# Performance work log

Hardware: AMD Instinct MI355X
Metric: run time of the kernel (lower is better)

## Reference

```python
import jax, jax.numpy as jnp
import numpy as np

N, F, H, EMB, R, E, B = 100000, 128, 128, 64, 3, 1600000, 1024


def rgcn_conv(x, edge_src, edge_dst, edge_type, W_rel, W_root, b):
    # PyG RGCNConv with aggr='mean': out_i = x_i @ W_root + b + sum_r mean_{j in N_r(i)} x_j @ W_r
    n = x.shape[0]
    r = W_rel.shape[0]
    xr = jnp.einsum('nf,rfh->rnh', x, W_rel)            # [R,N,H] per-relation transform
    msg = xr[edge_type, edge_src]                       # [E,H] gather per edge
    seg = edge_type.astype(jnp.int32) * n + edge_dst    # fused (rel, dst) segment id
    agg = jax.ops.segment_sum(msg, seg, num_segments=r * n).reshape(r, n, -1)
    cnt = jax.ops.segment_sum(jnp.ones((msg.shape[0],), msg.dtype), seg, num_segments=r * n)
    cnt = cnt.reshape(r, n, 1)
    agg = agg / jnp.maximum(cnt, 1.0)
    return agg.sum(0) + x @ W_root + b


def setup_inputs() -> dict:
    key = jax.random.key(0)
    ks = jax.random.split(key, 16)
    s = 0.05
    return {
        'x': jax.random.normal(ks[0], (N, F), jnp.float32),
        'edge_src': jax.random.randint(ks[1], (E,), 0, N, jnp.int32),
        'edge_dst': jax.random.randint(ks[2], (E,), 0, N, jnp.int32),
        'edge_type': jax.random.randint(ks[3], (E,), 0, R, jnp.int32),
        'edge_attr': jax.random.uniform(ks[4], (E, 2), jnp.float32),
        'nest': jax.random.randint(ks[5], (B,), 0, N, jnp.int32),
        'food': jax.random.randint(ks[6], (B,), 0, N, jnp.int32),
        'W_rel1': jax.random.normal(ks[7], (R, F, H), jnp.float32) * s,
        'W_root1': jax.random.normal(ks[8], (F, H), jnp.float32) * s,
        'b1': jnp.zeros((H,), jnp.float32),
        'W_rel2': jax.random.normal(ks[9], (R, H, EMB), jnp.float32) * s,
        'W_root2': jax.random.normal(ks[10], (H, EMB), jnp.float32) * s,
        'b2': jnp.zeros((EMB,), jnp.float32),
        'fc_W': jax.random.normal(ks[11], (2 * EMB, H), jnp.float32) * s,
        'fc_b': jnp.zeros((H,), jnp.float32),
    }


def reference(x, edge_src, edge_dst, edge_type, edge_attr, nest, food,
              W_rel1, W_root1, b1, W_rel2, W_root2, b2, fc_W, fc_b):
    # distance binning (computed in the original forward but unused downstream)
    d = edge_attr[:, 0]
    dmin, dmax = d.min(), d.max()
    bin_size = (dmax - dmin) / 3
    binned = jnp.clip(jnp.floor((d - dmin) / bin_size), 0, 2)
    del binned

    h1 = jax.nn.relu(rgcn_conv(x, edge_src, edge_dst, edge_type, W_rel1, W_root1, b1))
    node = rgcn_conv(h1, edge_src, edge_dst, edge_type, W_rel2, W_root2, b2)  # [N,EMB]
    pair = jnp.concatenate([node[nest], node[food]], axis=-1)  # [B, 2*EMB]
    return jnp.tanh(pair @ fc_W + fc_b)
```

## Files before the change

kernel.cpp:

```cpp
#include <hip/hip_runtime.h>
#include <stdint.h>

typedef unsigned short u16;
typedef __attribute__((ext_vector_type(8))) short short8;
typedef __attribute__((ext_vector_type(4))) float f32x4;
typedef __attribute__((ext_vector_type(2))) float f32x2;
typedef __attribute__((ext_vector_type(4))) unsigned int u32x4;

#define N_NODES 100000
#define RREL    3
#define NEDGE   1600000
#define NPAIR   1024
#define NSEG    (RREL * N_NODES)

#define EPB   4096
#define NBLK  ((NEDGE + EPB - 1) / EPB)
#define DPB   512
#define NBIN  ((N_NODES + DPB - 1) / DPB)
#define LSEG  (DPB * RREL)
#define CAP   12288

#define PREP_TW   384
#define PREP_CAST (N_NODES * 128 / 4 / 256)

__device__ __forceinline__ float bflo(unsigned int u) {
    union { unsigned int u; float f; } c; c.u = u << 16; return c.f;
}
__device__ __forceinline__ float bfhi(unsigned int u) {
    union { unsigned int u; float f; } c; c.u = u & 0xffff0000u; return c.f;
}
__device__ __forceinline__ u16 f2bf(float f) {
    union { float f; unsigned int u; } c; c.f = f;
    unsigned int u = c.u;
    u += 0x7fffu + ((u >> 16) & 1u);
    return (u16)(u >> 16);
}

__device__ __forceinline__ void async_copy16(const u16* g, u16* l) {
    __builtin_amdgcn_global_load_lds(
        (const __attribute__((address_space(1))) unsigned int*)g,
        (__attribute__((address_space(3))) unsigned int*)l,
        16, 0, 0);
}

__global__ __launch_bounds__(256) void prep_kernel(const int* __restrict__ es,
                                                   const int* __restrict__ ed,
                                                   const int* __restrict__ et,
                                                   int* __restrict__ gpos,
                                                   unsigned int* __restrict__ binned,
                                                   const float* __restrict__ x,
                                                   u16* __restrict__ xb,
                                                   const float* __restrict__ Wrel1,
                                                   const float* __restrict__ Wroot1,
                                                   const float* __restrict__ Wrel2,
                                                   const float* __restrict__ Wroot2,
                                                   u16* __restrict__ Wt1,
                                                   u16* __restrict__ Wt2) {
    __shared__ int h[NBIN];
    __shared__ int base[NBIN];
    int b = blockIdx.x, t = threadIdx.x;
    if (b < NBLK) {
        for (int i = t; i < NBIN; i += 256) h[i] = 0;
        __syncthreads();
        int e0 = b * EPB;
        int e1 = e0 + EPB; if (e1 > NEDGE) e1 = NEDGE;
        for (int i = e0 + t; i < e1; i += 256)
            atomicAdd(&h[ed[i] >> 9], 1);
        __syncthreads();
        for (int i = t; i < NBIN; i += 256) {
            int c = h[i];
            base[i] = c ? atomicAdd(&gpos[i], c) : 0;
            h[i] = 0;
        }
        __syncthreads();
        for (int i = e0 + t; i < e1; i += 256) {
            int d = ed[i];
            int bin = d >> 9;
            unsigned int pk = ((unsigned int)es[i] << 11) | (unsigned int)((d & 511) * 3 + et[i]);
            int off = atomicAdd(&h[bin], 1);
            binned[(size_t)bin * CAP + base[bin] + off] = pk;
        }
    } else if (b < NBLK + PREP_TW) {
        int idx = (b - NBLK) * 256 + t;
        if (idx < 128 * 512) {
            int n = idx >> 9, k = idx & 511;
            float v = (k < 384) ? Wrel1[(size_t)k * 128 + n] : Wroot1[(size_t)(k - 384) * 128 + n];
            Wt1[idx] = f2bf(v);
        } else {
            int j = idx - 128 * 512;
            if (j < 256 * 128) {
                int n = j >> 7, k = j & 127;
                float v = (n < 192) ? Wrel2[((size_t)(n >> 6) * 128 + k) * 64 + (n & 63)]
                                    : Wroot2[(size_t)k * 64 + (n - 192)];
                Wt2[j] = f2bf(v);
            }
        }
    } else {
        int i = (b - NBLK - PREP_TW) * 256 + t;
        f32x4 v = __builtin_nontemporal_load(&((const f32x4*)x)[i]);
        uint2 o;
        o.x = ((unsigned int)f2bf(v.y) << 16) | (unsigned int)f2bf(v.x);
        o.y = ((unsigned int)f2bf(v.w) << 16) | (unsigned int)f2bf(v.z);
        ((uint2*)xb)[i] = o;
    }
}

__global__ __launch_bounds__(256) void p4_finalize(const unsigned int* __restrict__ binned,
                                                   const int* __restrict__ gpos,
                                                   int* __restrict__ seg_start,
                                                   int* __restrict__ cnt,
                                                   int* __restrict__ sorted_src) {
    __shared__ int h[LSEG];
    __shared__ int cur[LSEG];
    __shared__ int wtot4[4];
    int t = threadIdx.x, bin = blockIdx.x;
    for (int i = t; i < LSEG; i += 256) h[i] = 0;
    __syncthreads();
    int eb = bin * CAP;
    int ee = eb + gpos[bin];
    for (int i = eb + t; i < ee; i += 256)
        atomicAdd(&h[binned[i] & 2047u], 1);
    __syncthreads();
    int i6 = t * 6;
    int s = 0;
    #pragma unroll
    for (int i = 0; i < 6; ++i) s += h[i6 + i];
    int lane = t & 63, wv = t >> 6;
    int incl = s;
    #pragma unroll
    for (int d = 1; d < 64; d <<= 1) { int v = __shfl_up(incl, d); if (lane >= d) incl += v; }
    if (lane == 63) wtot4[wv] = incl;
    __syncthreads();
    int wpre = 0;
    #pragma unroll
    for (int i = 0; i < 4; ++i) if (i < wv) wpre += wtot4[i];
    int run = wpre + incl - s;
    int segbase = bin * LSEG;
    #pragma unroll
    for (int i = 0; i < 6; ++i) {
        int ls = i6 + i;
        int c = h[ls];
        int seg = segbase + ls;
        if (seg < NSEG) { seg_start[seg] = eb + run; cnt[seg] = c; }
        cur[ls] = run;
        run += c;
    }
    __syncthreads();
    for (int i = eb + t; i < ee; i += 256) {
        unsigned int u = binned[i];
        int ls = (int)(u & 2047u);
        int p = atomicAdd(&cur[ls], 1);
        sorted_src[eb + p] = (int)(u >> 11);
    }
}

__global__ __launch_bounds__(256) void mark_nodes(const int* __restrict__ nest,
                                                  const int* __restrict__ food,
                                                  const int* __restrict__ seg_start,
                                                  const int* __restrict__ cnt,
                                                  const int* __restrict__ sorted_src,
                                                  int* __restrict__ flag) {
    int slot = blockIdx.x * 256 + threadIdx.x;
    if (slot >= NPAIR * 2) return;
    int p = slot >> 1, side = slot & 1;
    int dst = side ? food[p] : nest[p];
    if ((unsigned)dst >= (unsigned)N_NODES) dst = 0;
    flag[dst] = 1;
    int tot = cnt[dst * 3] + cnt[dst * 3 + 1] + cnt[dst * 3 + 2];
    int st = seg_start[dst * 3];
    for (int i = 0; i < tot; ++i)
        flag[sorted_src[st + i]] = 1;
}

__global__ __launch_bounds__(256) void compact_nodes(const int* __restrict__ flag,
                                                     int* __restrict__ ncnt,
                                                     int* __restrict__ list,
                                                     int* __restrict__ map) {
    int n = blockIdx.x * 256 + threadIdx.x;
    if (n >= N_NODES) return;
    if (flag[n]) {
        int idx = atomicAdd(ncnt, 1);
        list[idx] = n;
        map[n] = idx;
    }
}

__global__ __launch_bounds__(512, 8) void fused_l1(const uint4* __restrict__ X4,
                                                   const u16* __restrict__ xb,
                                                   const int* __restrict__ seg_start,
                                                   const int* __restrict__ cnt,
                                                   const int* __restrict__ sorted_src,
                                                   const u16* __restrict__ Wt1,
                                                   const float* __restrict__ b1,
                                                   const int* __restrict__ list,
                                                   const int* __restrict__ ncnt,
                                                   u16* __restrict__ h1c) {
    const int nc = *ncnt;
    const int bm  = blockIdx.x * 32;
    if (bm >= nc) return;
    __shared__ __align__(16) u16 Aagg[32 * 392];
    __shared__ __align__(16) u16 Aroot[32 * 32];
    __shared__ __align__(16) u16 Bs[128 * 32];
    const int t = threadIdx.x;
    const int w = t >> 6, l = t & 63;
    const int q4 = l >> 4, ql = l & 15;
    const int qid = w * 4 + q4;
    const int shbase = q4 * 16;

    int cArr[3], stArr[3];
    #pragma unroll
    for (int sp = 0; sp < 3; ++sp) {
        int seg_local = sp * 32 + qid;
        int n_loc = seg_local / 3, rel = seg_local - n_loc * 3;
        int nid = list[bm + n_loc];
        cArr[sp]  = cnt[nid * 3 + rel];
        stArr[sp] = seg_start[nid * 3 + rel];
    }
    #pragma unroll 1
    for (int sp = 0; sp < 3; ++sp) {
        int seg_local = sp * 32 + qid;
        int c  = cArr[sp];
        int st = stArr[sp];

        float a0 = 0.f, a1 = 0.f, a2 = 0.f, a3 = 0.f,
              a4 = 0.f, a5 = 0.f, a6 = 0.f, a7 = 0.f;

        for (int base = 0; base < c; base += 16) {
            int rem = c - base;
            int ii  = (ql < rem) ? ql : (rem - 1);
            int idxv = sorted_src[st + base + ii];
            int lim = (rem < 16) ? rem : 16;
            for (int j = 0; j < lim; j += 4) {
                int e1 = j + 1, e2 = j + 2, e3 = j + 3;
                float w1 = (e1 < lim) ? 1.f : 0.f;
                float w2 = (e2 < lim) ? 1.f : 0.f;
                float w3 = (e3 < lim) ? 1.f : 0.f;
                int s0 = __shfl(idxv, shbase + j);
                int s1 = __shfl(idxv, shbase + ((e1 < lim) ? e1 : 0));
                int s2 = __shfl(idxv, shbase + ((e2 < lim) ? e2 : 0));
                int s3 = __shfl(idxv, shbase + ((e3 < lim) ? e3 : 0));
                uint4 v0 = X4[(size_t)s0 * 16 + ql];
                uint4 v1 = X4[(size_t)s1 * 16 + ql];
                uint4 v2 = X4[(size_t)s2 * 16 + ql];
                uint4 v3 = X4[(size_t)s3 * 16 + ql];
                a0 += bflo(v0.x);               a1 += bfhi(v0.x);
                a2 += bflo(v0.y);               a3 += bfhi(v0.y);
                a4 += bflo(v0.z);               a5 += bfhi(v0.z);
                a6 += bflo(v0.w);               a7 += bfhi(v0.w);
                a0 = fmaf(w1, bflo(v1.x), a0);  a1 = fmaf(w1, bfhi(v1.x), a1);
                a2 = fmaf(w1, bflo(v1.y), a2);  a3 = fmaf(w1, bfhi(v1.y), a3);
                a4 = fmaf(w1, bflo(v1.z), a4);  a5 = fmaf(w1, bfhi(v1.z), a5);
                a6 = fmaf(w1, bflo(v1.w), a6);  a7 = fmaf(w1, bfhi(v1.w), a7);
                a0 = fmaf(w2, bflo(v2.x), a0);  a1 = fmaf(w2, bfhi(v2.x), a1);
                a2 = fmaf(w2, bflo(v2.y), a2);  a3 = fmaf(w2, bfhi(v2.y), a3);
                a4 = fmaf(w2, bflo(v2.z), a4);  a5 = fmaf(w2, bfhi(v2.z), a5);
                a6 = fmaf(w2, bflo(v2.w), a6);  a7 = fmaf(w2, bfhi(v2.w), a7);
                a0 = fmaf(w3, bflo(v3.x), a0);  a1 = fmaf(w3, bfhi(v3.x), a1);
                a2 = fmaf(w3, bflo(v3.y), a2);  a3 = fmaf(w3, bfhi(v3.y), a3);
                a4 = fmaf(w3, bflo(v3.z), a4);  a5 = fmaf(w3, bfhi(v3.z), a5);
                a6 = fmaf(w3, bflo(v3.w), a6);  a7 = fmaf(w3, bfhi(v3.w), a7);
            }
        }
        float sc = 1.0f / (float)(c > 0 ? c : 1);
        u32x4 o;
        o.x = ((unsigned int)f2bf(a1 * sc) << 16) | (unsigned int)f2bf(a0 * sc);
        o.y = ((unsigned int)f2bf(a3 * sc) << 16) | (unsigned int)f2bf(a2 * sc);
        o.z = ((unsigned int)f2bf(a5 * sc) << 16) | (unsigned int)f2bf(a4 * sc);
        o.w = ((unsigned int)f2bf(a7 * sc) << 16) | (unsigned int)f2bf(a6 * sc);
        int n_loc = seg_local / 3;
        int rel   = seg_local - n_loc * 3;
        *(u32x4*)&Aagg[n_loc * 392 + rel * 128 + ql * 8] = o;
    }
    __syncthreads();

    const int wm = w >> 2, wn = w & 3;
    const int q = l >> 4, lm = l & 15;
    f32x4 acc[2] = {};
    const int br  = t >> 2;
    const int bc4 = (t & 3) * 8;

    for (int kt = 0; kt < 16; ++kt) {
        const int k0 = kt * 32;
        __syncthreads();
        async_copy16(Wt1 + (size_t)br * 512 + k0 + bc4, &Bs[br * 32 + bc4]);
        if (kt >= 12 && w < 2) {
            async_copy16(xb + (size_t)list[bm + br] * 128 + (k0 - 384) + bc4, &Aroot[br * 32 + bc4]);
        }
        __syncthreads();
        short8 fa;
        if (kt < 12) fa = *(const short8*)&Aagg[(wm * 16 + lm) * 392 + k0 + q * 8];
        else         fa = *(const short8*)&Aroot[(wm * 16 + lm) * 32 + q * 8];
        #pragma unroll
        for (int ni = 0; ni < 2; ++ni) {
            short8 fb = *(const short8*)&Bs[(wn * 32 + ni * 16 + lm) * 32 + q * 8];
            acc[ni] = __builtin_amdgcn_mfma_f32_16x16x32_bf16(fa, fb, acc[ni], 0, 0, 0);
        }
    }
    #pragma unroll
    for (int ni = 0; ni < 2; ++ni) {
        int gc = wn * 32 + ni * 16 + lm;
        float bv = b1[gc];
        #pragma unroll
        for (int rg = 0; rg < 4; ++rg) {
            int gr = bm + wm * 16 + q * 4 + rg;
            float v = fmaxf(acc[ni][rg] + bv, 0.0f);
            h1c[(size_t)gr * 128 + gc] = f2bf(v);
        }
    }
}

__global__ __launch_bounds__(256) void gemm2_c(const u16* __restrict__ h1c,
                                               const u16* __restrict__ Wt2,
                                               const float* __restrict__ b2,
                                               const int* __restrict__ ncnt,
                                               u16* __restrict__ Pc,
                                               float* __restrict__ nodec) {
    const int nc = *ncnt;
    const int bm = blockIdx.x * 64;
    if (bm >= nc) return;
    __shared__ __align__(16) u16 As[64 * 32];
    __shared__ __align__(16) u16 Bs[256 * 32];
    const int t = threadIdx.x;
    const int w = t >> 6, l = t & 63;
    const int wn = w;
    const int q = l >> 4, lm = l & 15;

    f32x4 acc[4][4] = {};
    const int ar = t >> 2;
    const int ac = (t & 3) * 8;

    int gr0 = bm + ar; if (gr0 >= nc) gr0 = nc - 1;

    for (int kt = 0; kt < 4; ++kt) {
        const int k0 = kt * 32;
        __syncthreads();
        async_copy16(h1c + (size_t)gr0 * 128 + k0 + ac, &As[ar * 32 + ac]);
        #pragma unroll
        for (int i = 0; i < 4; ++i)
            async_copy16(Wt2 + (size_t)(i * 64 + ar) * 128 + k0 + ac,
                         &Bs[(i * 64 + ar) * 32 + ac]);
        __syncthreads();
        short8 fa[4], fb[4];
        #pragma unroll
        for (int mi = 0; mi < 4; ++mi)
            fa[mi] = *(const short8*)&As[(mi * 16 + lm) * 32 + q * 8];
        #pragma unroll
        for (int ni = 0; ni < 4; ++ni)
            fb[ni] = *(const short8*)&Bs[(wn * 64 + ni * 16 + lm) * 32 + q * 8];
        #pragma unroll
        for (int mi = 0; mi < 4; ++mi)
            #pragma unroll
            for (int ni = 0; ni < 4; ++ni)
                acc[mi][ni] = __builtin_amdgcn_mfma_f32_16x16x32_bf16(
                    fa[mi], fb[ni], acc[mi][ni], 0, 0, 0);
    }
    #pragma unroll
    for (int mi = 0; mi < 4; ++mi) {
        #pragma unroll
        for (int ni = 0; ni < 4; ++ni) {
            int gc = wn * 64 + ni * 16 + lm;
            float bv = (gc >= 192) ? b2[gc - 192] : 0.0f;
            #pragma unroll
            for (int rg = 0; rg < 4; ++rg) {
                int gr = bm + mi * 16 + q * 4 + rg;
                if (gr < nc) {
                    float v = acc[mi][ni][rg] + bv;
                    if (gc < 192) Pc[(size_t)gr * 192 + gc] = f2bf(v);
                    else          nodec[(size_t)gr * 64 + (gc - 192)] = v;
                }
            }
        }
    }
}

__global__ __launch_bounds__(256) void seg_pair(const u16* __restrict__ Pc,
                                                const int* __restrict__ seg_start,
                                                const int* __restrict__ cnt,
                                                const int* __restrict__ sorted_src,
                                                const float* __restrict__ nodec,
                                                const int* __restrict__ map,
                                                const int* __restrict__ nest,
                                                const int* __restrict__ food,
                                                float* __restrict__ pairbuf) {
    int lane = threadIdx.x & 63;
    int q4 = lane >> 4, ql = lane & 15;
    int e  = ql >> 3;
    int fl = ql & 7;
    int slot = ((blockIdx.x * 256 + threadIdx.x) >> 6) * 4 + q4;
    int p = slot >> 1, side = slot & 1;
    int dst = side ? food[p] : nest[p];
    if ((unsigned)dst >= (unsigned)N_NODES) dst = 0;
    int shbase = q4 * 16;

    int c0 = cnt[dst * 3 + 0], c1 = cnt[dst * 3 + 1], c2 = cnt[dst * 3 + 2];
    int st = seg_start[dst * 3 + 0];
    int c01 = c0 + c1, tot = c01 + c2;
    float r0 = c0 ? 1.0f / (float)c0 : 0.0f;
    float r1 = c1 ? 1.0f / (float)c1 : 0.0f;
    float r2 = c2 ? 1.0f / (float)c2 : 0.0f;

    const f32x4* np = (const f32x4*)(nodec + (size_t)map[dst] * 64 + fl * 8);
    f32x4 z0 = *np;
    f32x4 z1 = *(np + 1);

    f32x2 d0 = {0.f,0.f}, d1 = {0.f,0.f}, d2 = {0.f,0.f}, d3 = {0.f,0.f};

    for (int base = 0; base < tot; base += 16) {
        int rem = tot - base;
        int ii  = (ql < rem) ? ql : 0;
        int idxv = sorted_src[st + base + ii];
        int lim = (rem < 16) ? rem : 16;

        uint4 v[8];
        #pragma unroll
        for (int k = 0; k < 8; ++k) {
            int jj = 2 * k + e;
            int sel = (jj < lim) ? jj : 0;
            int s = __shfl(idxv, shbase + sel);
            int ge = base + sel;
            int rel = (ge >= c0) + (ge >= c01);
            v[k] = *(const uint4*)(Pc + (size_t)map[s] * 192 + rel * 64 + fl * 8);
        }
        #pragma unroll
        for (int k = 0; k < 8; ++k) {
            int jj = 2 * k + e;
            int ge = base + jj;
            float wr = (jj < lim) ? ((ge < c0) ? r0 : ((ge < c01) ? r1 : r2)) : 0.0f;
            f32x2 wv = {wr, wr};
            d0 += wv * (f32x2){bflo(v[k].x), bfhi(v[k].x)};
            d1 += wv * (f32x2){bflo(v[k].y), bfhi(v[k].y)};
            d2 += wv * (f32x2){bflo(v[k].z), bfhi(v[k].z)};
            d3 += wv * (f32x2){bflo(v[k].w), bfhi(v[k].w)};
        }
    }
    d0.x += __shfl_xor(d0.x, 8); d0.y += __shfl_xor(d0.y, 8);
    d1.x += __shfl_xor(d1.x, 8); d1.y += __shfl_xor(d1.y, 8);
    d2.x += __shfl_xor(d2.x, 8); d2.y += __shfl_xor(d2.y, 8);
    d3.x += __shfl_xor(d3.x, 8); d3.y += __shfl_xor(d3.y, 8);
    if (e == 0) {
        f32x4 o0 = {z0.x + d0.x, z0.y + d0.y, z0.z + d1.x, z0.w + d1.y};
        f32x4 o1 = {z1.x + d2.x, z1.y + d2.y, z1.z + d3.x, z1.w + d3.y};
        f32x4* op = (f32x4*)(pairbuf + (size_t)p * 128 + side * 64 + fl * 8);
        *op       = o0;
        *(op + 1) = o1;
    }
}

__global__ __launch_bounds__(128) void pair_mlp(const float* __restrict__ pairbuf,
                                                const float* __restrict__ fcW,
                                                const float* __restrict__ fcb,
                                                float* __restrict__ out) {
    int p = blockIdx.x;
    int t = threadIdx.x;
    __shared__ float pv[128];
    pv[t] = pairbuf[(size_t)p * 128 + t];
    __syncthreads();
    float s = fcb[t];
    #pragma unroll 4
    for (int k = 0; k < 128; ++k)
        s += pv[k] * fcW[k * 128 + t];
    out[(size_t)p * 128 + t] = tanhf(s);
}

extern "C" void kernel_launch(void* const* d_in, const int* in_sizes, int n_in,
                              void* d_out, int out_size, void* d_ws, size_t ws_size,
                              hipStream_t stream) {
    const float* x    = (const float*)d_in[0];
    const int* esrc   = (const int*)d_in[1];
    const int* edst   = (const int*)d_in[2];
    const int* etyp   = (const int*)d_in[3];
    const int* nest   = (const int*)d_in[5];
    const int* food   = (const int*)d_in[6];
    const float* Wrel1  = (const float*)d_in[7];
    const float* Wroot1 = (const float*)d_in[8];
    const float* b1     = (const float*)d_in[9];
    const float* Wrel2  = (const float*)d_in[10];
    const float* Wroot2 = (const float*)d_in[11];
    const float* b2     = (const float*)d_in[12];
    const float* fcW    = (const float*)d_in[13];
    const float* fcb    = (const float*)d_in[14];
    float* out = (float*)d_out;

    char* ws = (char*)d_ws;
    size_t off = 0;
    auto alloc_b = [&](size_t bytes) -> void* {
        void* p = ws + off;
        off += (bytes + 255) & ~(size_t)255;
        return p;
    };
    int* gpos        = (int*)alloc_b((size_t)NBIN * 4);
    unsigned int* bn = (unsigned int*)alloc_b((size_t)NBIN * CAP * 4);
    int* seg_start   = (int*)alloc_b((size_t)NSEG * 4);
    int* cnt         = (int*)alloc_b((size_t)NSEG * 4);
    int* sorted_src  = (int*)alloc_b((size_t)NBIN * CAP * 4);
    u16* Wt1         = (u16*)alloc_b((size_t)128 * 512 * 2);
    u16* Wt2         = (u16*)alloc_b((size_t)256 * 128 * 2);
    u16* xb          = (u16*)alloc_b((size_t)N_NODES * 128 * 2);
    u16* Pc          = (u16*)alloc_b((size_t)N_NODES * 192 * 2);
    u16* h1c         = (u16*)alloc_b((size_t)N_NODES * 128 * 2);
    float* nodec     = (float*)alloc_b((size_t)N_NODES * 64 * 4);
    float* pairbuf   = (float*)alloc_b((size_t)NPAIR * 128 * 4);
    int* ncnt        = (int*)alloc_b(4);
    int* flag        = (int*)alloc_b((size_t)N_NODES * 4);
    int* list        = (int*)alloc_b((size_t)N_NODES * 4);
    size_t zspan     = (size_t)((char*)(list + N_NODES) - (char*)ncnt);
    int* map         = (int*)alloc_b((size_t)N_NODES * 4);

    hipMemsetAsync(gpos, 0, (size_t)NBIN * 4, stream);
    hipMemsetAsync(ncnt, 0, zspan, stream);

    prep_kernel<<<NBLK + PREP_TW + PREP_CAST, 256, 0, stream>>>(
        esrc, edst, etyp, gpos, bn, x, xb, Wrel1, Wroot1, Wrel2, Wroot2, Wt1, Wt2);

    p4_finalize<<<NBIN, 256, 0, stream>>>(bn, gpos, seg_start, cnt, sorted_src);

    mark_nodes<<<(NPAIR * 2 + 255) / 256, 256, 0, stream>>>(
        nest, food, seg_start, cnt, sorted_src, flag);
    compact_nodes<<<(N_NODES + 255) / 256, 256, 0, stream>>>(flag, ncnt, list, map);

    fused_l1<<<N_NODES / 32, 512, 0, stream>>>(
        (const uint4*)xb, xb, seg_start, cnt, sorted_src, Wt1, b1, list, ncnt, h1c);

    gemm2_c<<<(N_NODES + 63) / 64, 256, 0, stream>>>(h1c, Wt2, b2, ncnt, Pc, nodec);
    seg_pair<<<(NPAIR * 2) / 16, 256, 0, stream>>>(
        Pc, seg_start, cnt, sorted_src, nodec, map, nest, food, pairbuf);

    pair_mlp<<<NPAIR, 128, 0, stream>>>(pairbuf, fcW, fcb, out);
}
```

Before: 271.5 us.

## Fuse node marking into finalize, pad bin counters, merge memsets, retune prep

Folds the mark_nodes kernel into p4_finalize: each bin block marks the pair nodes it owns, using its shared-memory histogram for the edge counts, which saves a launch. It also spaces the global bin counters 16 ints apart to reduce atomic contention, and reorders the workspace so a single memset clears the counters and the flag and list buffers. Edges per binning block drop from 4096 to 1024, and each cast thread now converts two vectors instead of one. Smaller edge blocks mean more global atomics per bin, and marking is now spread across 196 blocks that each loop over all 2048 slots.

```diff
diff --git a/kernel.cpp b/kernel.cpp
--- a/kernel.cpp
+++ b/kernel.cpp
@@ -13,15 +13,16 @@
 #define NPAIR   1024
 #define NSEG    (RREL * N_NODES)
 
-#define EPB   4096
+#define EPB   1024
 #define NBLK  ((NEDGE + EPB - 1) / EPB)
 #define DPB   512
 #define NBIN  ((N_NODES + DPB - 1) / DPB)
 #define LSEG  (DPB * RREL)
 #define CAP   12288
+#define GSTR  16
 
 #define PREP_TW   384
-#define PREP_CAST (N_NODES * 128 / 4 / 256)
+#define PREP_CAST (N_NODES * 128 / 8 / 256)
 
 __device__ __forceinline__ float bflo(unsigned int u) {
     union { unsigned int u; float f; } c; c.u = u << 16; return c.f;
@@ -69,7 +70,7 @@
         __syncthreads();
         for (int i = t; i < NBIN; i += 256) {
             int c = h[i];
-            base[i] = c ? atomicAdd(&gpos[i], c) : 0;
+            base[i] = c ? atomicAdd(&gpos[i * GSTR], c) : 0;
             h[i] = 0;
         }
         __syncthreads();
@@ -96,20 +97,27 @@
             }
         }
     } else {
-        int i = (b - NBLK - PREP_TW) * 256 + t;
-        f32x4 v = __builtin_nontemporal_load(&((const f32x4*)x)[i]);
-        uint2 o;
-        o.x = ((unsigned int)f2bf(v.y) << 16) | (unsigned int)f2bf(v.x);
-        o.y = ((unsigned int)f2bf(v.w) << 16) | (unsigned int)f2bf(v.z);
-        ((uint2*)xb)[i] = o;
+        int i0 = (b - NBLK - PREP_TW) * 512 + t;
+        f32x4 v0 = __builtin_nontemporal_load(&((const f32x4*)x)[i0]);
+        f32x4 v1 = __builtin_nontemporal_load(&((const f32x4*)x)[i0 + 256]);
+        uint2 o0, o1;
+        o0.x = ((unsigned int)f2bf(v0.y) << 16) | (unsigned int)f2bf(v0.x);
+        o0.y = ((unsigned int)f2bf(v0.w) << 16) | (unsigned int)f2bf(v0.z);
+        o1.x = ((unsigned int)f2bf(v1.y) << 16) | (unsigned int)f2bf(v1.x);
+        o1.y = ((unsigned int)f2bf(v1.w) << 16) | (unsigned int)f2bf(v1.z);
+        ((uint2*)xb)[i0]       = o0;
+        ((uint2*)xb)[i0 + 256] = o1;
     }
 }
 
 __global__ __launch_bounds__(256) void p4_finalize(const unsigned int* __restrict__ binned,
                                                    const int* __restrict__ gpos,
+                                                   const int* __restrict__ nest,
+                                                   const int* __restrict__ food,
                                                    int* __restrict__ seg_start,
                                                    int* __restrict__ cnt,
-                                                   int* __restrict__ sorted_src) {
+                                                   int* __restrict__ sorted_src,
+                                                   int* __restrict__ flag) {
     __shared__ int h[LSEG];
     __shared__ int cur[LSEG];
     __shared__ int wtot4[4];
@@ -117,7 +125,7 @@
     for (int i = t; i < LSEG; i += 256) h[i] = 0;
     __syncthreads();
     int eb = bin * CAP;
-    int ee = eb + gpos[bin];
+    int ee = eb + gpos[bin * GSTR];
     for (int i = eb + t; i < ee; i += 256)
         atomicAdd(&h[binned[i] & 2047u], 1);
     __syncthreads();
@@ -152,24 +160,20 @@
         int p = atomicAdd(&cur[ls], 1);
         sorted_src[eb + p] = (int)(u >> 11);
     }
-}
-
-__global__ __launch_bounds__(256) void mark_nodes(const int* __restrict__ nest,
-                                                  const int* __restrict__ food,
-                                                  const int* __restrict__ seg_start,
-                                                  const int* __restrict__ cnt,
-                                                  const int* __restrict__ sorted_src,
-                                                  int* __restrict__ flag) {
-    int slot = blockIdx.x * 256 + threadIdx.x;
-    if (slot >= NPAIR * 2) return;
-    int p = slot >> 1, side = slot & 1;
-    int dst = side ? food[p] : nest[p];
-    if ((unsigned)dst >= (unsigned)N_NODES) dst = 0;
-    flag[dst] = 1;
-    int tot = cnt[dst * 3] + cnt[dst * 3 + 1] + cnt[dst * 3 + 2];
-    int st = seg_start[dst * 3];
-    for (int i = 0; i < tot; ++i)
-        flag[sorted_src[st + i]] = 1;
+    __syncthreads();
+    for (int sl = t; sl < NPAIR * 2; sl += 256) {
+        int p = sl >> 1, side = sl & 1;
+        int dst = side ? food[p] : nest[p];
+        if ((unsigned)dst >= (unsigned)N_NODES) dst = 0;
+        if ((dst >> 9) == bin) {
+            flag[dst] = 1;
+            int ls0 = (dst & 511) * 3;
+            int tot = h[ls0] + h[ls0 + 1] + h[ls0 + 2];
+            int st0 = seg_start[dst * 3];
+            for (int i = 0; i < tot; ++i)
+                flag[sorted_src[st0 + i]] = 1;
+        }
+    }
 }
 
 __global__ __launch_bounds__(256) void compact_nodes(const int* __restrict__ flag,
@@ -488,7 +492,12 @@
         off += (bytes + 255) & ~(size_t)255;
         return p;
     };
-    int* gpos        = (int*)alloc_b((size_t)NBIN * 4);
+    int* gpos        = (int*)alloc_b((size_t)NBIN * GSTR * 4);
+    int* ncnt        = (int*)alloc_b(4);
+    int* flag        = (int*)alloc_b((size_t)N_NODES * 4);
+    int* list        = (int*)alloc_b((size_t)N_NODES * 4);
+    size_t zspan     = (size_t)((char*)(list + N_NODES) - (char*)gpos);
+    int* map         = (int*)alloc_b((size_t)N_NODES * 4);
     unsigned int* bn = (unsigned int*)alloc_b((size_t)NBIN * CAP * 4);
     int* seg_start   = (int*)alloc_b((size_t)NSEG * 4);
     int* cnt         = (int*)alloc_b((size_t)NSEG * 4);
@@ -500,22 +509,14 @@
     u16* h1c         = (u16*)alloc_b((size_t)N_NODES * 128 * 2);
     float* nodec     = (float*)alloc_b((size_t)N_NODES * 64 * 4);
     float* pairbuf   = (float*)alloc_b((size_t)NPAIR * 128 * 4);
-    int* ncnt        = (int*)alloc_b(4);
-    int* flag        = (int*)alloc_b((size_t)N_NODES * 4);
-    int* list        = (int*)alloc_b((size_t)N_NODES * 4);
-    size_t zspan     = (size_t)((char*)(list + N_NODES) - (char*)ncnt);
-    int* map         = (int*)alloc_b((size_t)N_NODES * 4);
-
-    hipMemsetAsync(gpos, 0, (size_t)NBIN * 4, stream);
-    hipMemsetAsync(ncnt, 0, zspan, stream);
+
+    hipMemsetAsync(gpos, 0, zspan, stream);
 
     prep_kernel<<<NBLK + PREP_TW + PREP_CAST, 256, 0, stream>>>(
         esrc, edst, etyp, gpos, bn, x, xb, Wrel1, Wroot1, Wrel2, Wroot2, Wt1, Wt2);
 
-    p4_finalize<<<NBIN, 256, 0, stream>>>(bn, gpos, seg_start, cnt, sorted_src);
-
-    mark_nodes<<<(NPAIR * 2 + 255) / 256, 256, 0, stream>>>(
-        nest, food, seg_start, cnt, sorted_src, flag);
+    p4_finalize<<<NBIN, 256, 0, stream>>>(bn, gpos, nest, food, seg_start, cnt, sorted_src, flag);
+
     compact_nodes<<<(N_NODES + 255) / 256, 256, 0, stream>>>(flag, ncnt, list, map);
 
     fused_l1<<<N_NODES / 32, 512, 0, stream>>>(
```

Result: slower. 290.5 us (+7.0%).
